# Kernel tuning notes

Hardware: AMD Instinct MI355X
Metric: run time of the kernel (lower is better)

Reference implementation:

```python
import itertools
import jax, jax.numpy as jnp
import numpy as np

N_FEATURES = 32
DEGREE = 3
BATCH = 32768


def poly_feature_indices(n_features: int, degree: int):
    indices = []
    for d in range(1, degree + 1):
        for combo in itertools.combinations_with_replacement(range(n_features), d):
            indices.append(combo)
    return indices


def padded_index_matrix(n_features: int, degree: int) -> np.ndarray:
    # Pad each monomial index tuple to length `degree` with the sentinel
    # index n_features, which points at a column of ones appended to x.
    idx_list = poly_feature_indices(n_features, degree)
    mat = np.full((len(idx_list), degree), n_features, dtype=np.int32)
    for i, tup in enumerate(idx_list):
        mat[i, : len(tup)] = tup
    return mat


def setup_inputs() -> dict:
    key = jax.random.key(0)
    k1, k2, k3 = jax.random.split(key, 3)
    n_poly = len(poly_feature_indices(N_FEATURES, DEGREE))  # 6544
    x = jax.random.normal(k1, (BATCH, N_FEATURES), dtype=jnp.float32)
    # nn.Linear(n_poly, 1) init scale
    bound = 1.0 / np.sqrt(n_poly)
    W = jax.random.uniform(k2, (1, n_poly), dtype=jnp.float32, minval=-bound, maxval=bound)
    b = jax.random.uniform(k3, (1,), dtype=jnp.float32, minval=-bound, maxval=bound)
    idx = jnp.asarray(padded_index_matrix(N_FEATURES, DEGREE))  # (n_poly, degree) int32
    return {"x": x, "W": W, "b": b, "idx": idx}


def reference(x, W, b, idx):
    # Append a ones column so the sentinel index acts as multiplicative identity.
    x_aug = jnp.concatenate([x, jnp.ones((x.shape[0], 1), dtype=x.dtype)], axis=1)
    # z[b, p] = prod_k x_aug[b, idx[p, k]]  -> (batch, n_poly)
    z = x_aug[:, idx[:, 0]]
    for k in range(1, idx.shape[1]):  # small fixed loop over degree
        z = z * x_aug[:, idx[:, k]]
    # Linear(n_poly, 1): z @ W.T + b
    return z @ W.T + b
```

## Files before the change

kernel.cpp:

```cpp
#include <hip/hip_runtime.h>


#define NPART 16
#define TOTAL3 5984

__device__ __forceinline__ constexpr int off2(int a, int b) {
    return 32 + 32 * a - (a * (a - 1)) / 2 + (b - a);
}

__device__ __forceinline__ constexpr int off3(int a, int b, int c) {
    constexpr int g3[32] = {
        0,    528,  1024, 1489, 1924, 2330, 2708, 3059,
        3384, 3684, 3960, 4213, 4444, 4654, 4844, 5015,
        5168, 5304, 5424, 5529, 5620, 5698, 5764, 5819,
        5864, 5900, 5928, 5949, 5964, 5974, 5980, 5983};
    return 560 + g3[a] + 32 * (b - a) - ((b * (b - 1)) / 2 - (a * (a - 1)) / 2) + (c - b);
}

__device__ __forceinline__ constexpr int cum3(int a, int b) {
    return off3(a, b, b) - 560;
}

__device__ __forceinline__ constexpr int owner_of(int a, int b) {
    return (cum3(a, b) * NPART) / TOTAL3;
}

template <int PART>
__device__ __forceinline__ void eval_part2(const float* __restrict__ Wl,
                                           const float (&x0)[32],
                                           const float (&x1)[32],
                                           float& r0, float& r1) {
    float a0 = 0.0f, a1 = 0.0f;
#pragma unroll
    for (int a = 0; a < 32; ++a) {
#pragma unroll
        for (int b = a; b < 32; ++b) {
            if (owner_of(a, b) == PART) {
                if (a == b) {
                    const float w1 = Wl[a];
                    a0 = __builtin_fmaf(w1, x0[a], a0);
                    a1 = __builtin_fmaf(w1, x1[a], a1);
                }
                const float w2 = Wl[off2(a, b)];
                float s0 = w2, s1 = w2;
#pragma unroll
                for (int c = b; c < 32; ++c) {
                    const float w = Wl[off3(a, b, c)];
                    s0 = __builtin_fmaf(w, x0[c], s0);
                    s1 = __builtin_fmaf(w, x1[c], s1);
                }
                a0 = __builtin_fmaf(x0[a] * x0[b], s0, a0);
                a1 = __builtin_fmaf(x1[a] * x1[b], s1, a1);
            }
        }
    }
    r0 = a0;
    r1 = a1;
}

__global__ __launch_bounds__(256) void PolyLinear_40218073760341_kernel(
    const float* __restrict__ X,
    const float* __restrict__ W,
    const float* __restrict__ Bp,
    float* __restrict__ out)
{
    const int part = blockIdx.x >> 6;
    const int tile = blockIdx.x & 63;
    const long rbase = (long)tile * 512 + threadIdx.x;

    __shared__ float Wl[6544];

    {
        const float4* Wg = (const float4*)W;
        float4* Wd = (float4*)Wl;
        for (int i = threadIdx.x; i < 1636; i += 256) Wd[i] = Wg[i];
    }

    float x0[32], x1[32];
    {
        const float4* p0 = (const float4*)(X + (rbase) * 32);
        const float4* p1 = (const float4*)(X + (rbase + 256) * 32);
#pragma unroll
        for (int i = 0; i < 8; ++i) {
            const float4 a = p0[i];
            x0[4 * i + 0] = a.x; x0[4 * i + 1] = a.y;
            x0[4 * i + 2] = a.z; x0[4 * i + 3] = a.w;
            const float4 b = p1[i];
            x1[4 * i + 0] = b.x; x1[4 * i + 1] = b.y;
            x1[4 * i + 2] = b.z; x1[4 * i + 3] = b.w;
        }
    }
    __syncthreads();

    float r0 = 0.0f, r1 = 0.0f;
#define EVAL_CASE(P) \
    case P: eval_part2<P>(Wl, x0, x1, r0, r1); break;
    switch (part) {
        EVAL_CASE(0)  EVAL_CASE(1)  EVAL_CASE(2)  EVAL_CASE(3)
        EVAL_CASE(4)  EVAL_CASE(5)  EVAL_CASE(6)  EVAL_CASE(7)
        EVAL_CASE(8)  EVAL_CASE(9)  EVAL_CASE(10) EVAL_CASE(11)
        EVAL_CASE(12) EVAL_CASE(13) EVAL_CASE(14) EVAL_CASE(15)
    }
#undef EVAL_CASE

    const float badd = (part == 0) ? Bp[0] : 0.0f;
    atomicAdd(&out[rbase], r0 + badd);
    atomicAdd(&out[rbase + 256], r1 + badd);
}

extern "C" void kernel_launch(void* const* d_in, const int* in_sizes, int n_in,
                              void* d_out, int out_size, void* d_ws, size_t ws_size,
                              hipStream_t stream) {
    const float* X  = (const float*)d_in[0];
    const float* W  = (const float*)d_in[1];
    const float* Bp = (const float*)d_in[2];
    float* out = (float*)d_out;

    const int rows = in_sizes[0] / 32;
    hipMemsetAsync(out, 0, (size_t)rows * sizeof(float), stream);
    const int grid = NPART * (rows / 512);
    PolyLinear_40218073760341_kernel<<<grid, 256, 0, stream>>>(X, W, Bp, out);
}
```

Baseline: 80.79 us.

## Split monomial partitions across waves within a block, reduce in shared memory

Instead of one block per (partition, row tile) with atomic accumulation into a memset output, each 512-thread block now handles 128 rows, and its 8 waves each evaluate one of 8 monomial partitions. Partial sums are reduced through shared memory and written directly, which removes the memset launch and the global atomics. The weight table is loaded into LDS once per 128 rows rather than once per 512 rows per partition. In exchange, a wave's work varies by which partition it holds inside a block, and each wave's unrolled code is larger with fewer parts.

```diff
diff --git a/kernel.cpp b/kernel.cpp
--- a/kernel.cpp
+++ b/kernel.cpp
@@ -1,7 +1,7 @@
 #include <hip/hip_runtime.h>
 
 
-#define NPART 16
+#define NPART 8
 #define TOTAL3 5984
 
 __device__ __forceinline__ constexpr int off2(int a, int b) {
@@ -58,28 +58,29 @@
     r1 = a1;
 }
 
-__global__ __launch_bounds__(256) void PolyLinear_40218073760341_kernel(
+__global__ __launch_bounds__(512) void PolyLinear_40218073760341_kernel(
     const float* __restrict__ X,
     const float* __restrict__ W,
     const float* __restrict__ Bp,
     float* __restrict__ out)
 {
-    const int part = blockIdx.x >> 6;
-    const int tile = blockIdx.x & 63;
-    const long rbase = (long)tile * 512 + threadIdx.x;
+    const int lane = threadIdx.x & 63;
+    const int wave = threadIdx.x >> 6;
+    const long base = (long)blockIdx.x * 128;
 
     __shared__ float Wl[6544];
+    __shared__ float partial[8][128];
 
     {
         const float4* Wg = (const float4*)W;
         float4* Wd = (float4*)Wl;
-        for (int i = threadIdx.x; i < 1636; i += 256) Wd[i] = Wg[i];
+        for (int i = threadIdx.x; i < 1636; i += 512) Wd[i] = Wg[i];
     }
 
     float x0[32], x1[32];
     {
-        const float4* p0 = (const float4*)(X + (rbase) * 32);
-        const float4* p1 = (const float4*)(X + (rbase + 256) * 32);
+        const float4* p0 = (const float4*)(X + (base + lane) * 32);
+        const float4* p1 = (const float4*)(X + (base + 64 + lane) * 32);
 #pragma unroll
         for (int i = 0; i < 8; ++i) {
             const float4 a = p0[i];
@@ -95,17 +96,22 @@
     float r0 = 0.0f, r1 = 0.0f;
 #define EVAL_CASE(P) \
     case P: eval_part2<P>(Wl, x0, x1, r0, r1); break;
-    switch (part) {
-        EVAL_CASE(0)  EVAL_CASE(1)  EVAL_CASE(2)  EVAL_CASE(3)
-        EVAL_CASE(4)  EVAL_CASE(5)  EVAL_CASE(6)  EVAL_CASE(7)
-        EVAL_CASE(8)  EVAL_CASE(9)  EVAL_CASE(10) EVAL_CASE(11)
-        EVAL_CASE(12) EVAL_CASE(13) EVAL_CASE(14) EVAL_CASE(15)
+    switch (wave) {
+        EVAL_CASE(0) EVAL_CASE(1) EVAL_CASE(2) EVAL_CASE(3)
+        EVAL_CASE(4) EVAL_CASE(5) EVAL_CASE(6) EVAL_CASE(7)
     }
 #undef EVAL_CASE
 
-    const float badd = (part == 0) ? Bp[0] : 0.0f;
-    atomicAdd(&out[rbase], r0 + badd);
-    atomicAdd(&out[rbase + 256], r1 + badd);
+    partial[wave][lane] = r0;
+    partial[wave][64 + lane] = r1;
+    __syncthreads();
+
+    if (threadIdx.x < 128) {
+        float r = Bp[0];
+#pragma unroll
+        for (int w = 0; w < 8; ++w) r += partial[w][threadIdx.x];
+        out[base + threadIdx.x] = r;
+    }
 }
 
 extern "C" void kernel_launch(void* const* d_in, const int* in_sizes, int n_in,
@@ -117,7 +123,6 @@
     float* out = (float*)d_out;
 
     const int rows = in_sizes[0] / 32;
-    hipMemsetAsync(out, 0, (size_t)rows * sizeof(float), stream);
-    const int grid = NPART * (rows / 512);
-    PolyLinear_40218073760341_kernel<<<grid, 256, 0, stream>>>(X, W, Bp, out);
+    const int grid = rows / 128;
+    PolyLinear_40218073760341_kernel<<<grid, 512, 0, stream>>>(X, W, Bp, out);
 }
```

Measured after the change: 72.31 us. 1.12x faster.
